# Kernel optimization log

Measured on AMD Instinct MI355X. Metric: run time of the kernel, lower is better.

The kernel has to match this reference:

```python
import jax, jax.numpy as jnp
import numpy as np

TOP_K = 4


def setup_inputs() -> dict:
    key = jax.random.key(0)
    ks = jax.random.split(key, 5)
    B, T, D = 2, 1024, 1024
    P, PD = 256, 32  # n_patterns, pattern_dim
    return {
        "x": jax.random.normal(ks[0], (B, T, D), dtype=jnp.float32),
        "hasher_w": jax.random.normal(ks[1], (PD, D), dtype=jnp.float32) * 0.03,
        "keys": jax.random.normal(ks[2], (P, PD), dtype=jnp.float32) * 0.1,
        "values_down": jax.random.normal(ks[3], (P, D, PD), dtype=jnp.float32) * 0.01,
        "values_up": jax.random.normal(ks[4], (P, PD, D), dtype=jnp.float32) * 0.01,
        "scale": jnp.full((1,), 0.1, dtype=jnp.float32),
    }


def reference(x, hasher_w, keys, values_down, values_up, scale):
    # h = hasher(x): [B,T,pattern_dim]
    h = jnp.einsum("btd,pd->btp", x, hasher_w)
    # similarity to pattern keys: [B,T,n_patterns]
    sim = jnp.einsum("btp,np->btn", h, keys)
    vals, idx = jax.lax.top_k(sim, TOP_K)          # [B,T,TOP_K]
    w = jax.nn.softmax(vals, axis=-1)              # softmax over the top-k scores
    out = jnp.zeros_like(x)
    for k in range(TOP_K):  # small fixed loop, matches original
        ik = idx[..., k]                            # [B,T] int32
        vd = values_down[ik]                        # [B,T,D,PD] gathered per-token
        vu = values_up[ik]                          # [B,T,PD,D]
        proj = jax.nn.silu(jnp.einsum("btd,btdp->btp", x, vd))
        o = jnp.einsum("btp,btpd->btd", proj, vu)
        out = out + o * w[..., k:k + 1]
    return x + out * scale
```

## Files before the change

kernel.cpp:

```cpp
#include <hip/hip_runtime.h>
#include <math.h>
#include <float.h>

#define DDIM 1024
#define PDIM 32
#define NPAT 256
#define TOPK 4
#define BLOCK 256
#define GT   16
#define DCH  256
#define NCH  4
#define RTPB 4

__global__ __launch_bounds__(BLOCK) void route_kernel(
    const float* __restrict__ x,
    const float* __restrict__ hasher_w,
    const float* __restrict__ keys,
    int*   __restrict__ tki,
    float* __restrict__ tkw,
    int ntok)
{
    __shared__ float P_s[RTPB][64 * 33];
    __shared__ float h_s[RTPB][32];

    const int tid  = threadIdx.x;
    const int wv   = tid >> 6;
    const int lane = tid & 63;
    const int tok  = min(blockIdx.x * RTPB + wv, ntok - 1);

    const float4* xrow = (const float4*)(x + (size_t)tok * DDIM);
    float4 xr[4];
    #pragma unroll
    for (int i = 0; i < 4; ++i) xr[i] = xrow[i * 64 + lane];

    float part[PDIM];
    #pragma unroll
    for (int pp = 0; pp < PDIM; ++pp) {
        const float4* wrow = (const float4*)(hasher_w + (size_t)pp * DDIM);
        float a = 0.f;
        #pragma unroll
        for (int i = 0; i < 4; ++i) {
            const float4 w4 = wrow[i * 64 + lane];
            a = fmaf(xr[i].x, w4.x, a); a = fmaf(xr[i].y, w4.y, a);
            a = fmaf(xr[i].z, w4.z, a); a = fmaf(xr[i].w, w4.w, a);
        }
        part[pp] = a;
    }

    float* P = P_s[wv];
    #pragma unroll
    for (int pp = 0; pp < PDIM; ++pp) P[lane * 33 + pp] = part[pp];
    __syncthreads();

    {
        const int pp = lane & 31, half = lane >> 5;
        float hsum = 0.f;
        #pragma unroll 8
        for (int i = 0; i < 32; ++i)
            hsum += P[(half * 32 + i) * 33 + pp];
        hsum += __shfl_xor(hsum, 32, 64);
        if (half == 0) h_s[wv][pp] = hsum;
    }
    __syncthreads();

    float4 h4[8];
    #pragma unroll
    for (int i = 0; i < 8; ++i) h4[i] = *(const float4*)&h_s[wv][i * 4];

    float sc0, sc1, sc2, sc3;
    {
        float sv[4];
        #pragma unroll
        for (int c = 0; c < 4; ++c) {
            const float4* kr = (const float4*)(keys + (size_t)(c * 64 + lane) * PDIM);
            float a = 0.f;
            #pragma unroll
            for (int i = 0; i < 8; ++i) {
                const float4 k4 = kr[i];
                a = fmaf(k4.x, h4[i].x, a); a = fmaf(k4.y, h4[i].y, a);
                a = fmaf(k4.z, h4[i].z, a); a = fmaf(k4.w, h4[i].w, a);
            }
            sv[c] = a;
        }
        sc0 = sv[0]; sc1 = sv[1]; sc2 = sv[2]; sc3 = sv[3];
    }

    float wval[TOPK]; int widx[TOPK];
    #pragma unroll
    for (int r = 0; r < TOPK; ++r) {
        float bv = sc0; int bc = 0;
        if (sc1 > bv) { bv = sc1; bc = 1; }
        if (sc2 > bv) { bv = sc2; bc = 2; }
        if (sc3 > bv) { bv = sc3; bc = 3; }
        int bidx = bc * 64 + lane;
        #pragma unroll
        for (int off = 1; off < 64; off <<= 1) {
            const float ov = __shfl_xor(bv, off, 64);
            const int   oi = __shfl_xor(bidx, off, 64);
            if (ov > bv || (ov == bv && oi < bidx)) { bv = ov; bidx = oi; }
        }
        wval[r] = bv; widx[r] = bidx;
        if ((bidx & 63) == lane) {
            const int c = bidx >> 6;
            if (c == 0) sc0 = -FLT_MAX;
            else if (c == 1) sc1 = -FLT_MAX;
            else if (c == 2) sc2 = -FLT_MAX;
            else sc3 = -FLT_MAX;
        }
    }

    if (lane == 0) {
        float m = wval[0];
        #pragma unroll
        for (int k = 1; k < TOPK; ++k) m = fmaxf(m, wval[k]);
        float s = 0.f, e[TOPK];
        #pragma unroll
        for (int k = 0; k < TOPK; ++k) { e[k] = expf(wval[k] - m); s += e[k]; }
        #pragma unroll
        for (int k = 0; k < TOPK; ++k) {
            tki[tok * TOPK + k] = widx[k];
            tkw[tok * TOPK + k] = e[k] / s;
        }
    }
}

__global__ __launch_bounds__(NPAT) void scanfill_kernel(
    const int* __restrict__ tki, const float* __restrict__ tkw,
    const float* __restrict__ scale_p,
    int* __restrict__ offs,
    int* __restrict__ etok, float* __restrict__ ew, int* __restrict__ slotof,
    int* __restrict__ tile2p, int* __restrict__ tilei,
    int nent, int maxt)
{
    __shared__ int s[NPAT];
    __shared__ int cur[NPAT];
    const int tid = threadIdx.x;

    cur[tid] = 0;
    __syncthreads();
    for (int e = tid; e < nent; e += NPAT) atomicAdd(&cur[tki[e]], 1);
    __syncthreads();

    const int v = cur[tid];
    s[tid] = v;
    __syncthreads();
    for (int off = 1; off < NPAT; off <<= 1) {
        int t = 0;
        if (tid >= off) t = s[tid - off];
        __syncthreads();
        s[tid] += t;
        __syncthreads();
    }
    const int incl = s[tid];
    offs[tid + 1] = incl;
    if (tid == 0) offs[0] = 0;
    cur[tid] = incl - v;
    __syncthreads();

    const int tc = (v + GT - 1) / GT;
    s[tid] = tc;
    __syncthreads();
    for (int off = 1; off < NPAT; off <<= 1) {
        int t = 0;
        if (tid >= off) t = s[tid - off];
        __syncthreads();
        s[tid] += t;
        __syncthreads();
    }
    const int toff = s[tid] - tc;
    for (int i = tid; i < maxt; i += NPAT) tile2p[i] = -1;
    __syncthreads();
    for (int i = 0; i < tc; ++i) { tile2p[toff + i] = tid; tilei[toff + i] = i; }

    const float sc = scale_p[0];
    for (int e = tid; e < nent; e += NPAT) {
        const int p = tki[e];
        const int slot = atomicAdd(&cur[p], 1);
        etok[slot] = e >> 2;
        ew[slot]   = tkw[e] * sc;
        slotof[e]  = slot;
    }
}

__global__ __launch_bounds__(BLOCK, 2) void proj_kernel(
    const float* __restrict__ x,
    const float* __restrict__ vd,
    const int* __restrict__ offs,
    const int* __restrict__ etok,
    const int* __restrict__ tile2p,
    const int* __restrict__ tilei,
    float* __restrict__ part,
    int nent)
{
    __shared__ float vd_s[DCH * PDIM];
    __shared__ float x_s[GT * DCH];
    __shared__ float red[4][8][68];
    __shared__ int   gt[GT];
    __shared__ int   gs[GT];

    const int tb  = blockIdx.x >> 2;
    const int c   = blockIdx.x & 3;
    const int p   = tile2p[tb];
    if (p < 0) return;
    const int tid = threadIdx.x;
    const int off0 = offs[p] + tilei[tb] * GT;
    const int gv   = min(GT, offs[p + 1] - off0);

    const float* vdp = vd + (size_t)p * DDIM * PDIM + (size_t)c * DCH * PDIM;
    #pragma unroll
    for (int k = 0; k < 8; ++k)
        ((float4*)vd_s)[k * 256 + tid] = ((const float4*)vdp)[k * 256 + tid];

    if (tid < GT) {
        if (tid < gv) { gt[tid] = etok[off0 + tid]; gs[tid] = off0 + tid; }
        else          { gt[tid] = etok[off0];       gs[tid] = nent; }
    }
    __syncthreads();

    #pragma unroll
    for (int k = 0; k < 4; ++k) {
        const int q  = k * 256 + tid;
        const int g  = q >> 6, fi = q & 63;
        ((float4*)x_s)[g * 64 + fi] =
            *(const float4*)(x + (size_t)gt[g] * DDIM + c * DCH + fi * 4);
    }
    __syncthreads();

    const int pp4 = tid & 7;
    const int seg = tid >> 3;
    float* partc = part + (size_t)c * (size_t)(nent + 1) * PDIM;

    float4 acc[GT];
    #pragma unroll
    for (int g = 0; g < GT; ++g) acc[g] = make_float4(0.f, 0.f, 0.f, 0.f);

    #pragma unroll
    for (int i4 = 0; i4 < 2; ++i4) {
        const int d0 = seg * 8 + i4 * 4;
        const float4 v0 = *(const float4*)&vd_s[(d0 + 0) * PDIM + pp4 * 4];
        const float4 v1 = *(const float4*)&vd_s[(d0 + 1) * PDIM + pp4 * 4];
        const float4 v2 = *(const float4*)&vd_s[(d0 + 2) * PDIM + pp4 * 4];
        const float4 v3 = *(const float4*)&vd_s[(d0 + 3) * PDIM + pp4 * 4];
        #pragma unroll
        for (int g = 0; g < GT; ++g) {
            const float4 xg = *(const float4*)&x_s[g * DCH + d0];
            acc[g].x = fmaf(xg.x, v0.x, acc[g].x);
            acc[g].y = fmaf(xg.x, v0.y, acc[g].y);
            acc[g].z = fmaf(xg.x, v0.z, acc[g].z);
            acc[g].w = fmaf(xg.x, v0.w, acc[g].w);
            acc[g].x = fmaf(xg.y, v1.x, acc[g].x);
            acc[g].y = fmaf(xg.y, v1.y, acc[g].y);
            acc[g].z = fmaf(xg.y, v1.z, acc[g].z);
            acc[g].w = fmaf(xg.y, v1.w, acc[g].w);
            acc[g].x = fmaf(xg.z, v2.x, acc[g].x);
            acc[g].y = fmaf(xg.z, v2.y, acc[g].y);
            acc[g].z = fmaf(xg.z, v2.z, acc[g].z);
            acc[g].w = fmaf(xg.z, v2.w, acc[g].w);
            acc[g].x = fmaf(xg.w, v3.x, acc[g].x);
            acc[g].y = fmaf(xg.w, v3.y, acc[g].y);
            acc[g].z = fmaf(xg.w, v3.z, acc[g].z);
            acc[g].w = fmaf(xg.w, v3.w, acc[g].w);
        }
    }

    #pragma unroll
    for (int g = 0; g < GT; ++g) {
        #pragma unroll
        for (int off = 8; off <= 32; off <<= 1) {
            acc[g].x += __shfl_xor(acc[g].x, off, 64);
            acc[g].y += __shfl_xor(acc[g].y, off, 64);
            acc[g].z += __shfl_xor(acc[g].z, off, 64);
            acc[g].w += __shfl_xor(acc[g].w, off, 64);
        }
    }
    const int wv = tid >> 6;
    if ((tid & 0x38) == 0) {
        #pragma unroll
        for (int g = 0; g < GT; ++g)
            *(float4*)&red[wv][pp4][g * 4] = acc[g];
    }
    __syncthreads();

    #pragma unroll
    for (int r = 0; r < 2; ++r) {
        const int idx = tid + r * BLOCK;
        const int g = idx >> 5, pp = idx & 31;
        const int q = pp >> 2, cmp = g * 4 + (pp & 3);
        const float s = red[0][q][cmp] + red[1][q][cmp]
                      + red[2][q][cmp] + red[3][q][cmp];
        partc[(size_t)gs[g] * PDIM + pp] = s;
    }
}

template <int MODE>
__global__ __launch_bounds__(BLOCK, 4) void up_kernel(
    const float* __restrict__ vu,
    const int* __restrict__ offs,
    const int* __restrict__ etok,
    const float* __restrict__ ew,
    const int* __restrict__ tile2p,
    const int* __restrict__ tilei,
    const float* __restrict__ part,
    float* __restrict__ dst,
    int nent)
{
    __shared__ float vu_s[PDIM * DCH];
    __shared__ float projT[PDIM][20];
    __shared__ int   gt[GT];
    __shared__ float gw[GT];
    __shared__ int   gs[GT];

    const int tb  = blockIdx.x >> 2;
    const int c   = blockIdx.x & 3;
    const int p   = tile2p[tb];
    if (p < 0) return;
    const int tid = threadIdx.x;
    const int off0 = offs[p] + tilei[tb] * GT;
    const int gv   = min(GT, offs[p + 1] - off0);

    const size_t PS = (size_t)(nent + 1) * PDIM;

    const float* vup = vu + (size_t)p * PDIM * DDIM + (size_t)c * DCH;
    #pragma unroll
    for (int k = 0; k < 8; ++k) {
        const int q  = k * 256 + tid;
        const int pp = q >> 6, fi = q & 63;
        *(float4*)&vu_s[pp * DCH + fi * 4] =
            *(const float4*)(vup + (size_t)pp * DDIM + fi * 4);
    }
    if (tid < GT) {
        if (tid < gv) {
            gt[tid] = etok[off0 + tid];
            gw[tid] = ew[off0 + tid];
            gs[tid] = off0 + tid;
        } else {
            gt[tid] = etok[off0]; gw[tid] = 0.f; gs[tid] = nent;
        }
    }
    __syncthreads();

    const int gq   = tid >> 6;
    const int lane = tid & 63;

    #pragma unroll
    for (int r = 0; r < 2; ++r) {
        const int idx = tid + r * BLOCK;
        const int g = idx >> 5, pp = idx & 31;
        const size_t row = (size_t)gs[g] * PDIM + pp;
        const float s = part[row] + part[PS + row]
                      + part[2 * PS + row] + part[3 * PS + row];
        const float pj = s / (1.f + expf(-s));
        projT[pp][g] = pj * gw[g];
    }
    __syncthreads();

    float4 o0 = make_float4(0.f, 0.f, 0.f, 0.f);
    float4 o1 = o0, o2 = o0, o3 = o0;
    #pragma unroll
    for (int pp = 0; pp < PDIM; ++pp) {
        const float4 pj4 = *(const float4*)&projT[pp][gq * 4];
        const float4 vu4 = *(const float4*)&vu_s[pp * DCH + lane * 4];
        o0.x = fmaf(pj4.x, vu4.x, o0.x); o0.y = fmaf(pj4.x, vu4.y, o0.y);
        o0.z = fmaf(pj4.x, vu4.z, o0.z); o0.w = fmaf(pj4.x, vu4.w, o0.w);
        o1.x = fmaf(pj4.y, vu4.x, o1.x); o1.y = fmaf(pj4.y, vu4.y, o1.y);
        o1.z = fmaf(pj4.y, vu4.z, o1.z); o1.w = fmaf(pj4.y, vu4.w, o1.w);
        o2.x = fmaf(pj4.z, vu4.x, o2.x); o2.y = fmaf(pj4.z, vu4.y, o2.y);
        o2.z = fmaf(pj4.z, vu4.z, o2.z); o2.w = fmaf(pj4.z, vu4.w, o2.w);
        o3.x = fmaf(pj4.w, vu4.x, o3.x); o3.y = fmaf(pj4.w, vu4.y, o3.y);
        o3.z = fmaf(pj4.w, vu4.z, o3.z); o3.w = fmaf(pj4.w, vu4.w, o3.w);
    }

    float4 ov[4] = {o0, o1, o2, o3};
    if (MODE == 0) {
        #pragma unroll
        for (int j = 0; j < 4; ++j)
            *(float4*)(dst + (size_t)gs[gq * 4 + j] * DDIM + c * DCH + lane * 4) = ov[j];
    } else {
        #pragma unroll
        for (int j = 0; j < 4; ++j) {
            const int g = gq * 4 + j;
            if (g < gv) {
                float* op = dst + (size_t)gt[g] * DDIM + c * DCH + lane * 4;
                atomicAdd(op + 0, ov[j].x);
                atomicAdd(op + 1, ov[j].y);
                atomicAdd(op + 2, ov[j].z);
                atomicAdd(op + 3, ov[j].w);
            }
        }
    }
}

__global__ __launch_bounds__(BLOCK) void combine_kernel(
    const float* __restrict__ x, const float* __restrict__ contrib,
    const int* __restrict__ slotof, float* __restrict__ out)
{
    __shared__ int sl[TOPK];
    const int t = blockIdx.x, tid = threadIdx.x;
    if (tid < TOPK) sl[tid] = slotof[t * TOPK + tid];
    __syncthreads();
    float4 r = ((const float4*)(x + (size_t)t * DDIM))[tid];
    #pragma unroll
    for (int k = 0; k < TOPK; ++k) {
        const float4 cv = ((const float4*)(contrib + (size_t)sl[k] * DDIM))[tid];
        r.x += cv.x; r.y += cv.y; r.z += cv.z; r.w += cv.w;
    }
    ((float4*)(out + (size_t)t * DDIM))[tid] = r;
}

extern "C" void kernel_launch(void* const* d_in, const int* in_sizes, int n_in,
                              void* d_out, int out_size, void* d_ws, size_t ws_size,
                              hipStream_t stream) {
    const float* x        = (const float*)d_in[0];
    const float* hasher_w = (const float*)d_in[1];
    const float* keys     = (const float*)d_in[2];
    const float* vd       = (const float*)d_in[3];
    const float* vu       = (const float*)d_in[4];
    const float* scale    = (const float*)d_in[5];
    float* out = (float*)d_out;

    const int ntok = in_sizes[0] / DDIM;
    if (ntok <= 0) return;
    const int nent = ntok * TOPK;
    const int maxt = (nent + GT - 1) / GT + NPAT;

    char* w = (char*)d_ws;
    const size_t o_offs = 1024;
    const size_t o_tki  = 2560;
    const size_t o_tkw  = o_tki  + (size_t)nent * 4;
    const size_t o_etok = o_tkw  + (size_t)nent * 4;
    const size_t o_ew   = o_etok + (size_t)nent * 4;
    const size_t o_slot = o_ew   + (size_t)nent * 4;
    const size_t o_t2p  = o_slot + (size_t)nent * 4;
    const size_t o_tli  = o_t2p  + (size_t)maxt * 4;
    const size_t o_part = (o_tli + (size_t)maxt * 4 + 255) & ~(size_t)255;
    const size_t partsz = (size_t)NCH * (size_t)(nent + 1) * PDIM * 4;
    const size_t o_ctb  = (o_part + partsz + 255) & ~(size_t)255;
    const size_t needPart    = o_ctb;
    const size_t needContrib = o_ctb + (size_t)(nent + 1) * DDIM * 4;

    int*   offs   = (int*)(w + o_offs);
    int*   tki    = (int*)(w + o_tki);
    float* tkw    = (float*)(w + o_tkw);
    int*   etok   = (int*)(w + o_etok);
    float* ew     = (float*)(w + o_ew);
    int*   slotof = (int*)(w + o_slot);
    int*   tile2p = (int*)(w + o_t2p);
    int*   tilei  = (int*)(w + o_tli);
    float* part   = (float*)(w + o_part);
    float* contrib= (float*)(w + o_ctb);

    const int rblocks = (ntok + RTPB - 1) / RTPB;
    hipLaunchKernelGGL(route_kernel, dim3(rblocks), dim3(BLOCK), 0, stream,
                       x, hasher_w, keys, tki, tkw, ntok);
    hipLaunchKernelGGL(scanfill_kernel, dim3(1), dim3(NPAT), 0, stream,
                       tki, tkw, scale, offs, etok, ew, slotof,
                       tile2p, tilei, nent, maxt);
    hipLaunchKernelGGL(proj_kernel, dim3(maxt * NCH), dim3(BLOCK), 0, stream,
                       x, vd, offs, etok, tile2p, tilei, part, nent);

    if (ws_size >= needContrib) {
        hipLaunchKernelGGL((up_kernel<0>), dim3(maxt * NCH), dim3(BLOCK), 0, stream,
                           vu, offs, etok, ew, tile2p, tilei, part, contrib, nent);
        hipLaunchKernelGGL(combine_kernel, dim3(ntok), dim3(BLOCK), 0, stream,
                           x, contrib, slotof, out);
    } else if (ws_size >= needPart) {
        hipMemcpyAsync(out, x, (size_t)ntok * DDIM * 4, hipMemcpyDeviceToDevice,
                       stream);
        hipLaunchKernelGGL((up_kernel<1>), dim3(maxt * NCH), dim3(BLOCK), 0, stream,
                           vu, offs, etok, ew, tile2p, tilei, part, out, nent);
    }
}
```

Baseline: 216.1 us.

## Split D into eight chunks and shrink per-thread work in proj and up kernels

Halves the D-chunk size from 256 to 128, doubling the number of blocks for the down-projection and up-projection kernels and halving their shared memory footprint. The proj kernel now gives each wave its own 4 tokens instead of having every thread cover all 16, which removes the cross-wave shared-memory reduction and a sync, and partial sums are written straight from registers. The up kernel assigns 2 tokens per thread instead of 4. Launch bounds are raised to target higher occupancy. In exchange the partial-sum buffer doubles and the up kernel now sums 8 partials per output, adding global memory traffic.

```diff
diff --git a/kernel.cpp b/kernel.cpp
--- a/kernel.cpp
+++ b/kernel.cpp
@@ -8,8 +8,8 @@
 #define TOPK 4
 #define BLOCK 256
 #define GT   16
-#define DCH  256
-#define NCH  4
+#define DCHP 128
+#define NCHP 8
 #define RTPB 4
 
 __global__ __launch_bounds__(BLOCK) void route_kernel(
@@ -182,7 +182,7 @@
     }
 }
 
-__global__ __launch_bounds__(BLOCK, 2) void proj_kernel(
+__global__ __launch_bounds__(BLOCK, 6) void proj_kernel(
     const float* __restrict__ x,
     const float* __restrict__ vd,
     const int* __restrict__ offs,
@@ -192,23 +192,22 @@
     float* __restrict__ part,
     int nent)
 {
-    __shared__ float vd_s[DCH * PDIM];
-    __shared__ float x_s[GT * DCH];
-    __shared__ float red[4][8][68];
+    __shared__ float vd_s[DCHP * PDIM];
+    __shared__ float x_s[GT * DCHP];
     __shared__ int   gt[GT];
     __shared__ int   gs[GT];
 
-    const int tb  = blockIdx.x >> 2;
-    const int c   = blockIdx.x & 3;
+    const int tb  = blockIdx.x >> 3;
+    const int c   = blockIdx.x & 7;
     const int p   = tile2p[tb];
     if (p < 0) return;
     const int tid = threadIdx.x;
     const int off0 = offs[p] + tilei[tb] * GT;
     const int gv   = min(GT, offs[p + 1] - off0);
 
-    const float* vdp = vd + (size_t)p * DDIM * PDIM + (size_t)c * DCH * PDIM;
-    #pragma unroll
-    for (int k = 0; k < 8; ++k)
+    const float* vdp = vd + (size_t)p * DDIM * PDIM + (size_t)c * DCHP * PDIM;
+    #pragma unroll
+    for (int k = 0; k < 4; ++k)
         ((float4*)vd_s)[k * 256 + tid] = ((const float4*)vdp)[k * 256 + tid];
 
     if (tid < GT) {
@@ -218,82 +217,73 @@
     __syncthreads();
 
     #pragma unroll
-    for (int k = 0; k < 4; ++k) {
+    for (int k = 0; k < 2; ++k) {
         const int q  = k * 256 + tid;
-        const int g  = q >> 6, fi = q & 63;
-        ((float4*)x_s)[g * 64 + fi] =
-            *(const float4*)(x + (size_t)gt[g] * DDIM + c * DCH + fi * 4);
-    }
-    __syncthreads();
-
-    const int pp4 = tid & 7;
-    const int seg = tid >> 3;
-    float* partc = part + (size_t)c * (size_t)(nent + 1) * PDIM;
-
-    float4 acc[GT];
-    #pragma unroll
-    for (int g = 0; g < GT; ++g) acc[g] = make_float4(0.f, 0.f, 0.f, 0.f);
-
-    #pragma unroll
-    for (int i4 = 0; i4 < 2; ++i4) {
-        const int d0 = seg * 8 + i4 * 4;
+        const int g  = q >> 5, fi = q & 31;
+        ((float4*)x_s)[g * 32 + fi] =
+            *(const float4*)(x + (size_t)gt[g] * DDIM + c * DCHP + fi * 4);
+    }
+    __syncthreads();
+
+    const int lane = tid & 63;
+    const int wv   = tid >> 6;
+    const int pp4  = lane & 7;
+    const int seg  = lane >> 3;
+
+    float4 acc[4];
+    #pragma unroll
+    for (int j = 0; j < 4; ++j) acc[j] = make_float4(0.f, 0.f, 0.f, 0.f);
+
+    #pragma unroll
+    for (int i4 = 0; i4 < 4; ++i4) {
+        const int d0 = seg * 16 + i4 * 4;
         const float4 v0 = *(const float4*)&vd_s[(d0 + 0) * PDIM + pp4 * 4];
         const float4 v1 = *(const float4*)&vd_s[(d0 + 1) * PDIM + pp4 * 4];
         const float4 v2 = *(const float4*)&vd_s[(d0 + 2) * PDIM + pp4 * 4];
         const float4 v3 = *(const float4*)&vd_s[(d0 + 3) * PDIM + pp4 * 4];
         #pragma unroll
-        for (int g = 0; g < GT; ++g) {
-            const float4 xg = *(const float4*)&x_s[g * DCH + d0];
-            acc[g].x = fmaf(xg.x, v0.x, acc[g].x);
-            acc[g].y = fmaf(xg.x, v0.y, acc[g].y);
-            acc[g].z = fmaf(xg.x, v0.z, acc[g].z);
-            acc[g].w = fmaf(xg.x, v0.w, acc[g].w);
-            acc[g].x = fmaf(xg.y, v1.x, acc[g].x);
-            acc[g].y = fmaf(xg.y, v1.y, acc[g].y);
-            acc[g].z = fmaf(xg.y, v1.z, acc[g].z);
-            acc[g].w = fmaf(xg.y, v1.w, acc[g].w);
-            acc[g].x = fmaf(xg.z, v2.x, acc[g].x);
-            acc[g].y = fmaf(xg.z, v2.y, acc[g].y);
-            acc[g].z = fmaf(xg.z, v2.z, acc[g].z);
-            acc[g].w = fmaf(xg.z, v2.w, acc[g].w);
-            acc[g].x = fmaf(xg.w, v3.x, acc[g].x);
-            acc[g].y = fmaf(xg.w, v3.y, acc[g].y);
-            acc[g].z = fmaf(xg.w, v3.z, acc[g].z);
-            acc[g].w = fmaf(xg.w, v3.w, acc[g].w);
-        }
-    }
-
-    #pragma unroll
-    for (int g = 0; g < GT; ++g) {
+        for (int j = 0; j < 4; ++j) {
+            const float4 xg = *(const float4*)&x_s[(wv * 4 + j) * DCHP + d0];
+            acc[j].x = fmaf(xg.x, v0.x, acc[j].x);
+            acc[j].y = fmaf(xg.x, v0.y, acc[j].y);
+            acc[j].z = fmaf(xg.x, v0.z, acc[j].z);
+            acc[j].w = fmaf(xg.x, v0.w, acc[j].w);
+            acc[j].x = fmaf(xg.y, v1.x, acc[j].x);
+            acc[j].y = fmaf(xg.y, v1.y, acc[j].y);
+            acc[j].z = fmaf(xg.y, v1.z, acc[j].z);
+            acc[j].w = fmaf(xg.y, v1.w, acc[j].w);
+            acc[j].x = fmaf(xg.z, v2.x, acc[j].x);
+            acc[j].y = fmaf(xg.z, v2.y, acc[j].y);
+            acc[j].z = fmaf(xg.z, v2.z, acc[j].z);
+            acc[j].w = fmaf(xg.z, v2.w, acc[j].w);
+            acc[j].x = fmaf(xg.w, v3.x, acc[j].x);
+            acc[j].y = fmaf(xg.w, v3.y, acc[j].y);
+            acc[j].z = fmaf(xg.w, v3.z, acc[j].z);
+            acc[j].w = fmaf(xg.w, v3.w, acc[j].w);
+        }
+    }
+
+    #pragma unroll
+    for (int j = 0; j < 4; ++j) {
         #pragma unroll
         for (int off = 8; off <= 32; off <<= 1) {
-            acc[g].x += __shfl_xor(acc[g].x, off, 64);
-            acc[g].y += __shfl_xor(acc[g].y, off, 64);
-            acc[g].z += __shfl_xor(acc[g].z, off, 64);
-            acc[g].w += __shfl_xor(acc[g].w, off, 64);
-        }
-    }
-    const int wv = tid >> 6;
-    if ((tid & 0x38) == 0) {
-        #pragma unroll
-        for (int g = 0; g < GT; ++g)
-            *(float4*)&red[wv][pp4][g * 4] = acc[g];
-    }
-    __syncthreads();
-
-    #pragma unroll
-    for (int r = 0; r < 2; ++r) {
-        const int idx = tid + r * BLOCK;
-        const int g = idx >> 5, pp = idx & 31;
-        const int q = pp >> 2, cmp = g * 4 + (pp & 3);
-        const float s = red[0][q][cmp] + red[1][q][cmp]
-                      + red[2][q][cmp] + red[3][q][cmp];
-        partc[(size_t)gs[g] * PDIM + pp] = s;
+            acc[j].x += __shfl_xor(acc[j].x, off, 64);
+            acc[j].y += __shfl_xor(acc[j].y, off, 64);
+            acc[j].z += __shfl_xor(acc[j].z, off, 64);
+            acc[j].w += __shfl_xor(acc[j].w, off, 64);
+        }
+    }
+
+    float* partc = part + (size_t)c * (size_t)(nent + 1) * PDIM;
+    if ((lane & 0x38) == 0) {
+        #pragma unroll
+        for (int j = 0; j < 4; ++j)
+            *(float4*)&partc[(size_t)gs[wv * 4 + j] * PDIM + pp4 * 4] = acc[j];
     }
 }
 
 template <int MODE>
-__global__ __launch_bounds__(BLOCK, 4) void up_kernel(
+__global__ __launch_bounds__(BLOCK, 6) void up_kernel(
     const float* __restrict__ vu,
     const int* __restrict__ offs,
     const int* __restrict__ etok,
@@ -304,14 +294,14 @@
     float* __restrict__ dst,
     int nent)
 {
-    __shared__ float vu_s[PDIM * DCH];
+    __shared__ float vu_s[PDIM * DCHP];
     __shared__ float projT[PDIM][20];
     __shared__ int   gt[GT];
     __shared__ float gw[GT];
     __shared__ int   gs[GT];
 
-    const int tb  = blockIdx.x >> 2;
-    const int c   = blockIdx.x & 3;
+    const int tb  = blockIdx.x >> 3;
+    const int c   = blockIdx.x & 7;
     const int p   = tile2p[tb];
     if (p < 0) return;
     const int tid = threadIdx.x;
@@ -320,12 +310,12 @@
 
     const size_t PS = (size_t)(nent + 1) * PDIM;
 
-    const float* vup = vu + (size_t)p * PDIM * DDIM + (size_t)c * DCH;
-    #pragma unroll
-    for (int k = 0; k < 8; ++k) {
+    const float* vup = vu + (size_t)p * PDIM * DDIM + (size_t)c * DCHP;
+    #pragma unroll
+    for (int k = 0; k < 4; ++k) {
         const int q  = k * 256 + tid;
-        const int pp = q >> 6, fi = q & 63;
-        *(float4*)&vu_s[pp * DCH + fi * 4] =
+        const int pp = q >> 5, fi = q & 31;
+        *(float4*)&vu_s[pp * DCHP + fi * 4] =
             *(const float4*)(vup + (size_t)pp * DDIM + fi * 4);
     }
     if (tid < GT) {
@@ -339,53 +329,49 @@
     }
     __syncthreads();
 
-    const int gq   = tid >> 6;
-    const int lane = tid & 63;
-
     #pragma unroll
     for (int r = 0; r < 2; ++r) {
         const int idx = tid + r * BLOCK;
         const int g = idx >> 5, pp = idx & 31;
         const size_t row = (size_t)gs[g] * PDIM + pp;
-        const float s = part[row] + part[PS + row]
-                      + part[2 * PS + row] + part[3 * PS + row];
+        float s = 0.f;
+        #pragma unroll
+        for (int i = 0; i < NCHP; ++i) s += part[i * PS + row];
         const float pj = s / (1.f + expf(-s));
         projT[pp][g] = pj * gw[g];
     }
     __syncthreads();
 
+    const int tg  = tid >> 5;
+    const int l32 = tid & 31;
+    const int g0 = tg * 2, g1 = tg * 2 + 1;
+
     float4 o0 = make_float4(0.f, 0.f, 0.f, 0.f);
-    float4 o1 = o0, o2 = o0, o3 = o0;
+    float4 o1 = o0;
     #pragma unroll
     for (int pp = 0; pp < PDIM; ++pp) {
-        const float4 pj4 = *(const float4*)&projT[pp][gq * 4];
-        const float4 vu4 = *(const float4*)&vu_s[pp * DCH + lane * 4];
-        o0.x = fmaf(pj4.x, vu4.x, o0.x); o0.y = fmaf(pj4.x, vu4.y, o0.y);
-        o0.z = fmaf(pj4.x, vu4.z, o0.z); o0.w = fmaf(pj4.x, vu4.w, o0.w);
-        o1.x = fmaf(pj4.y, vu4.x, o1.x); o1.y = fmaf(pj4.y, vu4.y, o1.y);
-        o1.z = fmaf(pj4.y, vu4.z, o1.z); o1.w = fmaf(pj4.y, vu4.w, o1.w);
-        o2.x = fmaf(pj4.z, vu4.x, o2.x); o2.y = fmaf(pj4.z, vu4.y, o2.y);
-        o2.z = fmaf(pj4.z, vu4.z, o2.z); o2.w = fmaf(pj4.z, vu4.w, o2.w);
-        o3.x = fmaf(pj4.w, vu4.x, o3.x); o3.y = fmaf(pj4.w, vu4.y, o3.y);
-        o3.z = fmaf(pj4.w, vu4.z, o3.z); o3.w = fmaf(pj4.w, vu4.w, o3.w);
-    }
-
-    float4 ov[4] = {o0, o1, o2, o3};
+        const float4 vu4 = *(const float4*)&vu_s[pp * DCHP + l32 * 4];
+        const float a = projT[pp][g0];
+        const float b = projT[pp][g1];
+        o0.x = fmaf(a, vu4.x, o0.x); o0.y = fmaf(a, vu4.y, o0.y);
+        o0.z = fmaf(a, vu4.z, o0.z); o0.w = fmaf(a, vu4.w, o0.w);
+        o1.x = fmaf(b, vu4.x, o1.x); o1.y = fmaf(b, vu4.y, o1.y);
+        o1.z = fmaf(b, vu4.z, o1.z); o1.w = fmaf(b, vu4.w, o1.w);
+    }
+
     if (MODE == 0) {
-        #pragma unroll
-        for (int j = 0; j < 4; ++j)
-            *(float4*)(dst + (size_t)gs[gq * 4 + j] * DDIM + c * DCH + lane * 4) = ov[j];
+        *(float4*)(dst + (size_t)gs[g0] * DDIM + c * DCHP + l32 * 4) = o0;
+        *(float4*)(dst + (size_t)gs[g1] * DDIM + c * DCHP + l32 * 4) = o1;
     } else {
-        #pragma unroll
-        for (int j = 0; j < 4; ++j) {
-            const int g = gq * 4 + j;
-            if (g < gv) {
-                float* op = dst + (size_t)gt[g] * DDIM + c * DCH + lane * 4;
-                atomicAdd(op + 0, ov[j].x);
-                atomicAdd(op + 1, ov[j].y);
-                atomicAdd(op + 2, ov[j].z);
-                atomicAdd(op + 3, ov[j].w);
-            }
+        if (g0 < gv) {
+            float* op = dst + (size_t)gt[g0] * DDIM + c * DCHP + l32 * 4;
+            atomicAdd(op + 0, o0.x); atomicAdd(op + 1, o0.y);
+            atomicAdd(op + 2, o0.z); atomicAdd(op + 3, o0.w);
+        }
+        if (g1 < gv) {
+            float* op = dst + (size_t)gt[g1] * DDIM + c * DCHP + l32 * 4;
+            atomicAdd(op + 0, o1.x); atomicAdd(op + 1, o1.y);
+            atomicAdd(op + 2, o1.z); atomicAdd(op + 3, o1.w);
         }
     }
 }
@@ -433,7 +419,7 @@
     const size_t o_t2p  = o_slot + (size_t)nent * 4;
     const size_t o_tli  = o_t2p  + (size_t)maxt * 4;
     const size_t o_part = (o_tli + (size_t)maxt * 4 + 255) & ~(size_t)255;
-    const size_t partsz = (size_t)NCH * (size_t)(nent + 1) * PDIM * 4;
+    const size_t partsz = (size_t)NCHP * (size_t)(nent + 1) * PDIM * 4;
     const size_t o_ctb  = (o_part + partsz + 255) & ~(size_t)255;
     const size_t needPart    = o_ctb;
     const size_t needContrib = o_ctb + (size_t)(nent + 1) * DDIM * 4;
@@ -455,18 +441,18 @@
     hipLaunchKernelGGL(scanfill_kernel, dim3(1), dim3(NPAT), 0, stream,
                        tki, tkw, scale, offs, etok, ew, slotof,
                        tile2p, tilei, nent, maxt);
-    hipLaunchKernelGGL(proj_kernel, dim3(maxt * NCH), dim3(BLOCK), 0, stream,
+    hipLaunchKernelGGL(proj_kernel, dim3(maxt * NCHP), dim3(BLOCK), 0, stream,
                        x, vd, offs, etok, tile2p, tilei, part, nent);
 
     if (ws_size >= needContrib) {
-        hipLaunchKernelGGL((up_kernel<0>), dim3(maxt * NCH), dim3(BLOCK), 0, stream,
+        hipLaunchKernelGGL((up_kernel<0>), dim3(maxt * NCHP), dim3(BLOCK), 0, stream,
                            vu, offs, etok, ew, tile2p, tilei, part, contrib, nent);
         hipLaunchKernelGGL(combine_kernel, dim3(ntok), dim3(BLOCK), 0, stream,
                            x, contrib, slotof, out);
     } else if (ws_size >= needPart) {
         hipMemcpyAsync(out, x, (size_t)ntok * DDIM * 4, hipMemcpyDeviceToDevice,
                        stream);
-        hipLaunchKernelGGL((up_kernel<1>), dim3(maxt * NCH), dim3(BLOCK), 0, stream,
+        hipLaunchKernelGGL((up_kernel<1>), dim3(maxt * NCHP), dim3(BLOCK), 0, stream,
                            vu, offs, etok, ew, tile2p, tilei, part, out, nent);
     }
 }
```

Measured after the change: 208.9 us. 1.03x faster.
